# Performance work log

Measured on AMD Instinct MI355X. Metric: run time of the kernel, lower is better.

Reference implementation:

```python
import jax, jax.numpy as jnp
import numpy as np

B, S, IN, E, H, NH = 32, 1024, 16, 128, 256, 4
DH = E // NH
EPS = 1e-5


def _ln(x, g, b):
    mu = jnp.mean(x, axis=-1, keepdims=True)
    var = jnp.mean(jnp.square(x - mu), axis=-1, keepdims=True)
    return (x - mu) * jax.lax.rsqrt(var + EPS) * g + b


def setup_inputs() -> dict:
    key = jax.random.key(0)
    ks = iter(jax.random.split(key, 32))
    n = lambda shape, s=0.02: jax.random.normal(next(ks), shape, jnp.float32) * s
    inp = {
        "x": jax.random.normal(next(ks), (B, S, IN), jnp.float32),
        "mask": jax.random.uniform(next(ks), (B, S), jnp.float32),
        "embed_w": n((E, IN)), "embed_b": jnp.zeros((E,), jnp.float32),
        # 3 encoder layers, params stacked on leading layer axis
        "in_proj_w": n((3, 3 * E, E)), "in_proj_b": jnp.zeros((3, 3 * E), jnp.float32),
        "out_w": n((3, E, E)), "out_b": jnp.zeros((3, E), jnp.float32),
        "ln1_g": jnp.ones((3, E), jnp.float32), "ln1_b": jnp.zeros((3, E), jnp.float32),
        "ln2_g": jnp.ones((3, E), jnp.float32), "ln2_b": jnp.zeros((3, E), jnp.float32),
        "ffn_w1": n((3, E, E)), "ffn_b1": jnp.zeros((3, E), jnp.float32),
        "ffn_w2": n((3, E, E)), "ffn_b2": jnp.zeros((3, E), jnp.float32),
        "cls_w1": n((H, E)), "cls_b1": jnp.zeros((H,), jnp.float32),
        "cls_w2": n((H, H)), "cls_b2": jnp.zeros((H,), jnp.float32),
        "cls_w3": n((H, H)), "cls_b3": jnp.zeros((H,), jnp.float32),
        "cls_w4": n((1, H)), "cls_b4": jnp.zeros((1,), jnp.float32),
    }
    return inp


def _encoder_layer(x, ipw, ipb, ow, ob, g1, b1, g2, b2, w1, fb1, w2, fb2):
    # PyTorch TransformerEncoderLayer, norm_first=False (post-norm), relu FFN
    qkv = x @ ipw.T + ipb                      # [B,S,3E]
    q, k, v = jnp.split(qkv, 3, axis=-1)
    q = q.reshape(B, S, NH, DH).transpose(0, 2, 1, 3)
    k = k.reshape(B, S, NH, DH).transpose(0, 2, 1, 3)
    v = v.reshape(B, S, NH, DH).transpose(0, 2, 1, 3)
    scores = jnp.einsum("bhqd,bhkd->bhqk", q, k) / np.sqrt(DH)  # naive O(S^2) math SDPA
    attn = jax.nn.softmax(scores, axis=-1)
    o = jnp.einsum("bhqk,bhkd->bhqd", attn, v)
    o = o.transpose(0, 2, 1, 3).reshape(B, S, E) @ ow.T + ob
    x = _ln(x + o, g1, b1)
    ff = jax.nn.relu(x @ w1.T + fb1) @ w2.T + fb2
    return _ln(x + ff, g2, b2)


def reference(x, mask, embed_w, embed_b, in_proj_w, in_proj_b, out_w, out_b,
              ln1_g, ln1_b, ln2_g, ln2_b, ffn_w1, ffn_b1, ffn_w2, ffn_b2,
              cls_w1, cls_b1, cls_w2, cls_b2, cls_w3, cls_b3, cls_w4, cls_b4):
    h = jax.nn.relu(x @ embed_w.T + embed_b)   # [B,S,E]
    for i in range(3):
        h = _encoder_layer(h, in_proj_w[i], in_proj_b[i], out_w[i], out_b[i],
                           ln1_g[i], ln1_b[i], ln2_g[i], ln2_b[i],
                           ffn_w1[i], ffn_b1[i], ffn_w2[i], ffn_b2[i])
    pooled = jnp.sum(h * mask[:, :, None], axis=1)  # [B,E] masked sum pool
    z = jax.nn.relu(pooled @ cls_w1.T + cls_b1)
    z = jax.nn.relu(z @ cls_w2.T + cls_b2)
    z = jax.nn.relu(z @ cls_w3.T + cls_b3)
    return jax.nn.sigmoid(z @ cls_w4.T + cls_b4)    # [B,1]
```

## Files before the change

### kernel.cpp

```cpp
#include <hip/hip_runtime.h>
#include <hip/hip_bf16.h>
#include <math.h>

#define B 32
#define S 1024
#define IN_DIM 16
#define E 128
#define NH 4
#define DH 32
#define HDIM 256
#define ROWS (B*S)
#define EPS 1e-5f

#define N_IPW (3*384*128)
#define N_SQ  (3*128*128)
#define NCVT ((N_IPW + 3*N_SQ) / 256)

typedef __bf16 bf16x8 __attribute__((ext_vector_type(8)));
typedef __bf16 bf16x4 __attribute__((ext_vector_type(4)));
typedef __bf16 bf16x2 __attribute__((ext_vector_type(2)));
typedef float f32x4 __attribute__((ext_vector_type(4)));
typedef float f32x16 __attribute__((ext_vector_type(16)));

#define MFMA16 __builtin_amdgcn_mfma_f32_16x16x32_bf16
#define MFMA32 __builtin_amdgcn_mfma_f32_32x32x16_bf16

union BF2U { bf16x2 b; unsigned int u; };
__device__ inline unsigned int pk2(float a, float b) {
    BF2U x; x.b[0] = (__bf16)a; x.b[1] = (__bf16)b; return x.u;
}

union U8 { bf16x8 v8; bf16x4 v4[2]; unsigned u4[4]; };
__device__ inline void st8(__bf16* p, bf16x8 v) {
    U8 u; u.v8 = v;
    *(bf16x4*)p = u.v4[0];
    *(bf16x4*)(p + 4) = u.v4[1];
}
__device__ inline bf16x8 ld8(const __bf16* p) {
    U8 u;
    u.v4[0] = *(const bf16x4*)p;
    u.v4[1] = *(const bf16x4*)(p + 4);
    return u.v8;
}

__global__ __launch_bounds__(256) void k_embedcvt(
        const float* __restrict__ ipw, const float* __restrict__ ow,
        const float* __restrict__ w1, const float* __restrict__ w2,
        __bf16* __restrict__ wbo,
        const float* __restrict__ x, const float* __restrict__ W,
        const float* __restrict__ bias, __bf16* __restrict__ hb)
{
    int t = threadIdx.x;
    if (blockIdx.x < NCVT) {
        int i = blockIdx.x * 256 + t;
        float v;
        if (i < N_IPW) v = ipw[i];
        else if (i < N_IPW + N_SQ) v = ow[i - N_IPW];
        else if (i < N_IPW + 2 * N_SQ) v = w1[i - N_IPW - N_SQ];
        else v = w2[i - N_IPW - 2 * N_SQ];
        wbo[i] = (__bf16)v;
        return;
    }
    int row0 = (blockIdx.x - NCVT) * 16;
    __shared__ float xs[16][16];
    xs[t >> 4][t & 15] = x[(row0 + (t >> 4)) * IN_DIM + (t & 15)];
    __syncthreads();
    int sub = t >> 7, tc = t & 127;
    float w[16];
#pragma unroll
    for (int i = 0; i < 16; ++i) w[i] = W[tc * 16 + i];
    float bb = bias[tc];
#pragma unroll
    for (int rr = 0; rr < 8; ++rr) {
        int lr = sub * 8 + rr;
        float acc = bb;
#pragma unroll
        for (int i = 0; i < 16; ++i) acc += xs[lr][i] * w[i];
        hb[(size_t)(row0 + lr) * E + tc] = (__bf16)fmaxf(acc, 0.f);
    }
}

__global__ __launch_bounds__(512, 2) void k_qkvattn(
        const __bf16* __restrict__ hb, const __bf16* __restrict__ Wip,
        const float* __restrict__ bip, __bf16* __restrict__ O)
{
    __shared__ __attribute__((aligned(16))) __bf16 Ksh[1024][36];
    __shared__ __attribute__((aligned(16))) __bf16 Vsh[32][1036];
    __shared__ __attribute__((aligned(16))) __bf16 Pm[8][32][36];

    int t = threadIdx.x, lane = t & 63, wv = t >> 6;
    int l15 = lane & 15, quad = lane >> 4;
    int l31 = lane & 31, hi = lane >> 5;
    int lb = ((blockIdx.x & 7) << 5) | (blockIdx.x >> 3);
    int half = lb & 1, bh = lb >> 1;
    int hh = bh & 3, b = bh >> 2;

    const __bf16* hpanel = hb + (size_t)b * S * E;

    const float qscale = 0.1767766952966369f * 1.4426950408889634f * 8388608.0f;
    const float C2 = 1065101558.0f;
    f32x16 cinit16, z16;
#pragma unroll
    for (int i = 0; i < 16; ++i) { cinit16[i] = C2; z16[i] = 0.f; }

    bf16x8 bQ[2][2];
    {
        bf16x8 bWq[8];
#pragma unroll
        for (int ch = 0; ch < 8; ++ch)
            bWq[ch] = *(const bf16x8*)&Wip[(size_t)(hh*32 + l31)*128 + ch*16 + hi*8];
        float bq = bip[hh*32 + l31];
#pragma unroll
        for (int qt = 0; qt < 2; ++qt) {
            int qrow0 = half*512 + wv*64 + qt*32;
            f32x16 aq = z16;
#pragma unroll
            for (int ch = 0; ch < 8; ++ch) {
                bf16x8 ah = *(const bf16x8*)&hpanel[(size_t)(qrow0 + l31)*128 + ch*16 + hi*8];
                aq = MFMA32(ah, bWq[ch], aq, 0, 0, 0);
            }
#pragma unroll
            for (int r = 0; r < 16; ++r) {
                int q = (r & 3) + 8*(r >> 2) + 4*hi;
                Pm[wv][q][l31] = (__bf16)((aq[r] + bq) * qscale);
            }
            __asm__ __volatile__("" ::: "memory");
            bQ[qt][0] = ld8(&Pm[wv][l31][hi*8]);
            bQ[qt][1] = ld8(&Pm[wv][l31][16 + hi*8]);
            __asm__ __volatile__("" ::: "memory");
        }
    }

    {
        bf16x8 bWk[2][4], bWv[2][4];
#pragma unroll
        for (int df = 0; df < 2; ++df)
#pragma unroll
            for (int kc = 0; kc < 4; ++kc) {
                bWk[df][kc] = *(const bf16x8*)&Wip[(size_t)(128 + hh*32 + df*16 + l15)*128 + kc*32 + quad*8];
                bWv[df][kc] = *(const bf16x8*)&Wip[(size_t)(256 + hh*32 + df*16 + l15)*128 + kc*32 + quad*8];
            }
        float bk0 = bip[128 + hh*32 + l15],  bk1 = bip[128 + hh*32 + 16 + l15];
        float bvb0 = bip[256 + hh*32 + l15], bvb1 = bip[256 + hh*32 + 16 + l15];
        int srow = wv*16 + l15;
        bf16x8 af[4], ag[4];
#pragma unroll
        for (int kc = 0; kc < 4; ++kc)
            af[kc] = *(const bf16x8*)&hpanel[(size_t)srow*128 + kc*32 + quad*8];
        const f32x4 z4 = {0.f, 0.f, 0.f, 0.f};
        for (int c = 0; c < 8; ++c) {
            if (c < 7) {
#pragma unroll
                for (int kc = 0; kc < 4; ++kc)
                    ag[kc] = *(const bf16x8*)&hpanel[(size_t)((c+1)*128 + srow)*128 + kc*32 + quad*8];
            }
            f32x4 k0 = z4, k1 = z4, v0 = z4, v1 = z4;
#pragma unroll
            for (int kc = 0; kc < 4; ++kc) {
                k0 = MFMA16(af[kc], bWk[0][kc], k0, 0, 0, 0);
                k1 = MFMA16(af[kc], bWk[1][kc], k1, 0, 0, 0);
                v0 = MFMA16(af[kc], bWv[0][kc], v0, 0, 0, 0);
                v1 = MFMA16(af[kc], bWv[1][kc], v1, 0, 0, 0);
            }
            int s0 = c*128 + wv*16 + quad*4;
#pragma unroll
            for (int r = 0; r < 4; ++r) {
                Ksh[s0 + r][l15]      = (__bf16)(k0[r] + bk0);
                Ksh[s0 + r][16 + l15] = (__bf16)(k1[r] + bk1);
            }
            uint2 u0, u1;
            u0.x = pk2(v0[0] + bvb0, v0[1] + bvb0);
            u0.y = pk2(v0[2] + bvb0, v0[3] + bvb0);
            u1.x = pk2(v1[0] + bvb1, v1[1] + bvb1);
            u1.y = pk2(v1[2] + bvb1, v1[3] + bvb1);
            *(uint2*)&Vsh[l15][s0] = u0;
            *(uint2*)&Vsh[16 + l15][s0] = u1;
#pragma unroll
            for (int kc = 0; kc < 4; ++kc) af[kc] = ag[kc];
        }
    }
    __syncthreads();

    bf16x8 vones;
#pragma unroll
    for (int j = 0; j < 8; ++j) vones[j] = (__bf16)1.0f;
    f32x16 o[2], ol[2];
    o[0] = z16; o[1] = z16; ol[0] = z16; ol[1] = z16;

    for (int c = 0; c < 16; ++c) {
        bf16x8 aK[2][2];
#pragma unroll
        for (int sub = 0; sub < 2; ++sub)
#pragma unroll
            for (int dh = 0; dh < 2; ++dh)
                aK[sub][dh] = ld8(&Ksh[c*64 + sub*32 + l31][dh*16 + hi*8]);
        bf16x8 bVf[4];
#pragma unroll
        for (int ch = 0; ch < 4; ++ch) {
            U8 u;
            const __bf16* vp = &Vsh[l31][c*64 + ch*16 + hi*4];
            u.v4[0] = *(const bf16x4*)vp;
            u.v4[1] = *(const bf16x4*)(vp + 8);
            bVf[ch] = u.v8;
        }
#pragma unroll
        for (int qt = 0; qt < 2; ++qt) {
#pragma unroll
            for (int sub = 0; sub < 2; ++sub) {
                f32x16 acc = cinit16;
                acc = MFMA32(aK[sub][0], bQ[qt][0], acc, 0, 0, 0);
                acc = MFMA32(aK[sub][1], bQ[qt][1], acc, 0, 0, 0);
#pragma unroll
                for (int g = 0; g < 2; ++g) {
                    U8 u;
#pragma unroll
                    for (int r = 0; r < 4; ++r) {
                        int ia = (int)acc[g*8 + 2*r];
                        int ib = (int)acc[g*8 + 2*r + 1];
                        u.u4[r] = __builtin_amdgcn_perm((unsigned)ib, (unsigned)ia, 0x07060302u);
                    }
                    bf16x8 ap = u.v8;
                    int ch = sub*2 + g;
                    o[qt]  = MFMA32(ap, bVf[ch], o[qt], 0, 0, 0);
                    ol[qt] = MFMA32(ap, vones,  ol[qt], 0, 0, 0);
                }
            }
        }
    }

#pragma unroll
    for (int qt = 0; qt < 2; ++qt)
#pragma unroll
        for (int r = 0; r < 16; ++r) {
            float linv = 1.f / ol[qt][r];
            int q = (r & 3) + 8*(r >> 2) + 4*hi;
            int row = half*512 + wv*64 + qt*32 + q;
            O[((size_t)(b * S) + row) * E + hh*32 + l31] = (__bf16)(o[qt][r] * linv);
        }
}

__global__ __launch_bounds__(512, 4) void k_layer2(const __bf16* __restrict__ t0b,
        const __bf16* __restrict__ Wo, const float* __restrict__ ob,
        const float* __restrict__ g1, const float* __restrict__ bt1,
        const __bf16* __restrict__ W1, const float* __restrict__ b1v,
        const __bf16* __restrict__ W2, const float* __restrict__ b2v,
        const float* __restrict__ g2, const float* __restrict__ bt2,
        __bf16* __restrict__ hb)
{
    __shared__ __attribute__((aligned(16))) __bf16 As[64][132];
    __shared__ __attribute__((aligned(16))) __bf16 Ws[128][132];
    __shared__ float red[2][64][2];
    int t = threadIdx.x;
    int m0 = blockIdx.x * 64;
    int arow = t >> 3, acol = (t & 7) * 16;
    int wrow = t >> 2, wcol = (t & 3) * 32;
    {
        const __bf16* Ap = t0b + (size_t)(m0 + arow) * 128 + acol;
#pragma unroll
        for (int j = 0; j < 2; ++j)
            st8(&As[arow][acol + j * 8], *(const bf16x8*)&Ap[j * 8]);
        const __bf16* Wp = Wo + (size_t)wrow * 128 + wcol;
#pragma unroll
        for (int j = 0; j < 4; ++j)
            st8(&Ws[wrow][wcol + j * 8], *(const bf16x8*)&Wp[j * 8]);
    }
    __syncthreads();
    int lane = t & 63, wv = t >> 6;
    int l15 = lane & 15, quad = lane >> 4;
    int nh = wv & 1, mh = wv >> 1;
    f32x4 acc[4];

#pragma unroll
    for (int i = 0; i < 4; ++i) acc[i] = (f32x4){0.f, 0.f, 0.f, 0.f};
#pragma unroll
    for (int kc = 0; kc < 4; ++kc) {
        bf16x8 aw[4], ba;
#pragma unroll
        for (int nc = 0; nc < 4; ++nc)
            aw[nc] = ld8(&Ws[nh * 64 + nc * 16 + l15][kc * 32 + quad * 8]);
        ba = ld8(&As[mh * 16 + l15][kc * 32 + quad * 8]);
#pragma unroll
        for (int nc = 0; nc < 4; ++nc)
            acc[nc] = MFMA16(aw[nc], ba, acc[nc], 0, 0, 0);
    }
    float s1 = 0.f, s2 = 0.f;
    int m = m0 + mh * 16 + l15;
#pragma unroll
    for (int nc = 0; nc < 4; ++nc) {
        float4 bv = *(const float4*)&ob[nh * 64 + nc * 16 + quad * 4];
        bf16x4 rv = *(const bf16x4*)&hb[(size_t)m * 128 + nh * 64 + nc * 16 + quad * 4];
        acc[nc][0] += bv.x + (float)rv[0];
        acc[nc][1] += bv.y + (float)rv[1];
        acc[nc][2] += bv.z + (float)rv[2];
        acc[nc][3] += bv.w + (float)rv[3];
#pragma unroll
        for (int i = 0; i < 4; ++i) {
            s1 += acc[nc][i];
            s2 += acc[nc][i] * acc[nc][i];
        }
    }
    s1 += __shfl_xor(s1, 16); s1 += __shfl_xor(s1, 32);
    s2 += __shfl_xor(s2, 16); s2 += __shfl_xor(s2, 32);
    if (quad == 0) {
        red[nh][mh * 16 + l15][0] = s1;
        red[nh][mh * 16 + l15][1] = s2;
    }
    __syncthreads();
    float mu, rs;
    {
        int r = mh * 16 + l15;
        float S1 = red[0][r][0] + red[1][r][0];
        float S2 = red[0][r][1] + red[1][r][1];
        mu = S1 * (1.f / 128.f);
        float var = S2 * (1.f / 128.f) - mu * mu;
        rs = rsqrtf(var + EPS);
    }
    bf16x4 res2[4];
#pragma unroll
    for (int nc = 0; nc < 4; ++nc) {
        float4 gv = *(const float4*)&g1[nh * 64 + nc * 16 + quad * 4];
        float4 bb = *(const float4*)&bt1[nh * 64 + nc * 16 + quad * 4];
        float o0 = (acc[nc][0] - mu) * rs * gv.x + bb.x;
        float o1 = (acc[nc][1] - mu) * rs * gv.y + bb.y;
        float o2 = (acc[nc][2] - mu) * rs * gv.z + bb.z;
        float o3 = (acc[nc][3] - mu) * rs * gv.w + bb.w;
        bf16x4 xb;
        xb[0] = (__bf16)o0; xb[1] = (__bf16)o1;
        xb[2] = (__bf16)o2; xb[3] = (__bf16)o3;
        res2[nc] = xb;
        *(bf16x4*)&As[mh * 16 + l15][nh * 64 + nc * 16 + quad * 4] = xb;
    }
    {
        const __bf16* Wp = W1 + (size_t)wrow * 128 + wcol;
#pragma unroll
        for (int j = 0; j < 4; ++j)
            st8(&Ws[wrow][wcol + j * 8], *(const bf16x8*)&Wp[j * 8]);
    }
    __syncthreads();

#pragma unroll
    for (int i = 0; i < 4; ++i) acc[i] = (f32x4){0.f, 0.f, 0.f, 0.f};
#pragma unroll
    for (int kc = 0; kc < 4; ++kc) {
        bf16x8 aw[4], ba;
#pragma unroll
        for (int nc = 0; nc < 4; ++nc)
            aw[nc] = ld8(&Ws[nh * 64 + nc * 16 + l15][kc * 32 + quad * 8]);
        ba = ld8(&As[mh * 16 + l15][kc * 32 + quad * 8]);
#pragma unroll
        for (int nc = 0; nc < 4; ++nc)
            acc[nc] = MFMA16(aw[nc], ba, acc[nc], 0, 0, 0);
    }
    __syncthreads();
#pragma unroll
    for (int nc = 0; nc < 4; ++nc) {
        float4 bv = *(const float4*)&b1v[nh * 64 + nc * 16 + quad * 4];
        float v0 = fmaxf(acc[nc][0] + bv.x, 0.f);
        float v1 = fmaxf(acc[nc][1] + bv.y, 0.f);
        float v2 = fmaxf(acc[nc][2] + bv.z, 0.f);
        float v3 = fmaxf(acc[nc][3] + bv.w, 0.f);
        uint2 u; u.x = pk2(v0, v1); u.y = pk2(v2, v3);
        *(uint2*)&As[mh * 16 + l15][nh * 64 + nc * 16 + quad * 4] = u;
    }
    {
        const __bf16* Wp = W2 + (size_t)wrow * 128 + wcol;
#pragma unroll
        for (int j = 0; j < 4; ++j)
            st8(&Ws[wrow][wcol + j * 8], *(const bf16x8*)&Wp[j * 8]);
    }
    __syncthreads();

#pragma unroll
    for (int i = 0; i < 4; ++i) acc[i] = (f32x4){0.f, 0.f, 0.f, 0.f};
#pragma unroll
    for (int kc = 0; kc < 4; ++kc) {
        bf16x8 aw[4], ba;
#pragma unroll
        for (int nc = 0; nc < 4; ++nc)
            aw[nc] = ld8(&Ws[nh * 64 + nc * 16 + l15][kc * 32 + quad * 8]);
        ba = ld8(&As[mh * 16 + l15][kc * 32 + quad * 8]);
#pragma unroll
        for (int nc = 0; nc < 4; ++nc)
            acc[nc] = MFMA16(aw[nc], ba, acc[nc], 0, 0, 0);
    }
    s1 = 0.f; s2 = 0.f;
#pragma unroll
    for (int nc = 0; nc < 4; ++nc) {
        float4 bv = *(const float4*)&b2v[nh * 64 + nc * 16 + quad * 4];
        acc[nc][0] += bv.x + (float)res2[nc][0];
        acc[nc][1] += bv.y + (float)res2[nc][1];
        acc[nc][2] += bv.z + (float)res2[nc][2];
        acc[nc][3] += bv.w + (float)res2[nc][3];
#pragma unroll
        for (int i = 0; i < 4; ++i) {
            s1 += acc[nc][i];
            s2 += acc[nc][i] * acc[nc][i];
        }
    }
    s1 += __shfl_xor(s1, 16); s1 += __shfl_xor(s1, 32);
    s2 += __shfl_xor(s2, 16); s2 += __shfl_xor(s2, 32);
    if (quad == 0) {
        red[nh][mh * 16 + l15][0] = s1;
        red[nh][mh * 16 + l15][1] = s2;
    }
    __syncthreads();
    {
        int r = mh * 16 + l15;
        float S1 = red[0][r][0] + red[1][r][0];
        float S2 = red[0][r][1] + red[1][r][1];
        mu = S1 * (1.f / 128.f);
        float var = S2 * (1.f / 128.f) - mu * mu;
        rs = rsqrtf(var + EPS);
    }
#pragma unroll
    for (int nc = 0; nc < 4; ++nc) {
        float4 gv = *(const float4*)&g2[nh * 64 + nc * 16 + quad * 4];
        float4 bb = *(const float4*)&bt2[nh * 64 + nc * 16 + quad * 4];
        float o0 = (acc[nc][0] - mu) * rs * gv.x + bb.x;
        float o1 = (acc[nc][1] - mu) * rs * gv.y + bb.y;
        float o2 = (acc[nc][2] - mu) * rs * gv.z + bb.z;
        float o3 = (acc[nc][3] - mu) * rs * gv.w + bb.w;
        uint2 u; u.x = pk2(o0, o1); u.y = pk2(o2, o3);
        *(uint2*)&hb[(size_t)m * 128 + nh * 64 + nc * 16 + quad * 4] = u;
    }
}

__global__ __launch_bounds__(128) void k_pool1(const __bf16* __restrict__ h,
        const float* __restrict__ mask, float* __restrict__ part)
{
    int bx = blockIdx.x;
    int b = bx >> 3, ch = bx & 7, t = threadIdx.x;
    float acc = 0.f;
    const __bf16* hp = h + (size_t)(b * S + ch * 128) * E + t;
    const float* mp = mask + b * S + ch * 128;
    for (int s = 0; s < 128; ++s) acc += (float)hp[(size_t)s * E] * mp[s];
    part[(size_t)bx * E + t] = acc;
}

__global__ __launch_bounds__(256) void k_head(const float* __restrict__ part,
        const float* __restrict__ cw1, const float* __restrict__ cb1,
        const float* __restrict__ cw2, const float* __restrict__ cb2,
        const float* __restrict__ cw3, const float* __restrict__ cb3,
        const float* __restrict__ cw4, const float* __restrict__ cb4,
        float* __restrict__ out)
{
    int b = blockIdx.x, t = threadIdx.x;
    __shared__ float p[128], za[256], zb[256];
    __shared__ float red4[4];
    if (t < 128) {
        float a = 0.f;
#pragma unroll
        for (int c = 0; c < 8; ++c) a += part[(size_t)(b * 8 + c) * 128 + t];
        p[t] = a;
    }
    __syncthreads();
    float a1 = cb1[t];
    for (int k = 0; k < 128; ++k) a1 += p[k] * cw1[t * 128 + k];
    za[t] = fmaxf(a1, 0.f);
    __syncthreads();
    float a2 = cb2[t];
    for (int k = 0; k < 256; ++k) a2 += za[k] * cw2[t * 256 + k];
    zb[t] = fmaxf(a2, 0.f);
    __syncthreads();
    float a3 = cb3[t];
    for (int k = 0; k < 256; ++k) a3 += zb[k] * cw3[t * 256 + k];
    float z3 = fmaxf(a3, 0.f);
    float prt = z3 * cw4[t];
#pragma unroll
    for (int o2 = 32; o2; o2 >>= 1) prt += __shfl_xor(prt, o2);
    if ((t & 63) == 0) red4[t >> 6] = prt;
    __syncthreads();
    if (t == 0) {
        float sum = red4[0] + red4[1] + red4[2] + red4[3] + cb4[0];
        out[b] = 1.f / (1.f + __expf(-sum));
    }
}

extern "C" void kernel_launch(void* const* d_in, const int* in_sizes, int n_in,
                              void* d_out, int out_size, void* d_ws, size_t ws_size,
                              hipStream_t stream)
{
    const float* x     = (const float*)d_in[0];
    const float* mask  = (const float*)d_in[1];
    const float* emb_w = (const float*)d_in[2];
    const float* emb_b = (const float*)d_in[3];
    const float* ipw   = (const float*)d_in[4];
    const float* ipb   = (const float*)d_in[5];
    const float* ow    = (const float*)d_in[6];
    const float* ob    = (const float*)d_in[7];
    const float* ln1g  = (const float*)d_in[8];
    const float* ln1b  = (const float*)d_in[9];
    const float* ln2g  = (const float*)d_in[10];
    const float* ln2b  = (const float*)d_in[11];
    const float* w1    = (const float*)d_in[12];
    const float* fb1   = (const float*)d_in[13];
    const float* w2    = (const float*)d_in[14];
    const float* fb2   = (const float*)d_in[15];
    const float* cw1   = (const float*)d_in[16];
    const float* cb1   = (const float*)d_in[17];
    const float* cw2   = (const float*)d_in[18];
    const float* cb2   = (const float*)d_in[19];
    const float* cw3   = (const float*)d_in[20];
    const float* cb3   = (const float*)d_in[21];
    const float* cw4   = (const float*)d_in[22];
    const float* cb4   = (const float*)d_in[23];

    char* p = (char*)d_ws;
    __bf16* hb   = (__bf16*)p;   p += (size_t)ROWS * E * 2;
    p += (size_t)ROWS * 256 * 2;
    p += (size_t)ROWS * 32 * 4 * 2 / 4;
    __bf16* t0b  = (__bf16*)p;   p += (size_t)ROWS * E * 2;
    __bf16* wb   = (__bf16*)p;   p += (size_t)(N_IPW + 3 * N_SQ) * 2;
    float* part  = (float*)p;    p += (size_t)B * 8 * E * 4;

    __bf16* wb_ipw = wb;
    __bf16* wb_ow  = wb + N_IPW;
    __bf16* wb_w1  = wb_ow + N_SQ;
    __bf16* wb_w2  = wb_w1 + N_SQ;

    k_embedcvt<<<NCVT + ROWS / 16, 256, 0, stream>>>(
        ipw, ow, w1, w2, wb, x, emb_w, emb_b, hb);
    for (int L = 0; L < 3; ++L) {
        k_qkvattn<<<B * NH * 2, 512, 0, stream>>>(
            hb, wb_ipw + (size_t)L * 384 * 128, ipb + L * 384, t0b);
        k_layer2<<<ROWS / 64, 512, 0, stream>>>(
            t0b, wb_ow + (size_t)L * 128 * 128, ob + L * 128,
            ln1g + L * E, ln1b + L * E,
            wb_w1 + (size_t)L * 128 * 128, fb1 + L * 128,
            wb_w2 + (size_t)L * 128 * 128, fb2 + L * 128,
            ln2g + L * E, ln2b + L * E, hb);
    }
    k_pool1<<<B * 8, 128, 0, stream>>>(hb, mask, part);
    k_head<<<B, 256, 0, stream>>>(part, cw1, cb1, cw2, cb2, cw3, cb3, cw4, cb4,
                                  (float*)d_out);
}
```

Before: 291.7 us.

## Double attention block threads, one query tile per wave, scalar row sums

The attention kernel now launches 1024 threads per block. Each of the 16 waves owns a single 32-row query tile instead of two, and the K/V projection loop splits across twice as many waves. The row-sum MFMA against a ones vector is replaced by a scalar accumulation of the probabilities plus a cross-lane shuffle and a small shared scratch. The Q staging buffer now reuses the Ksh region, which adds a barrier. The pooling kernel is vectorised with 8-wide bf16 loads and a shared-memory reduction. This trades per-wave register pressure and MFMA work for more waves per CU, with a risk of occupancy limits from the 1024-thread launch bound.

```diff
diff --git a/kernel.cpp b/kernel.cpp
--- a/kernel.cpp
+++ b/kernel.cpp
@@ -80,13 +80,13 @@
     }
 }
 
-__global__ __launch_bounds__(512, 2) void k_qkvattn(
+__global__ __launch_bounds__(1024, 4) void k_qkvattn(
         const __bf16* __restrict__ hb, const __bf16* __restrict__ Wip,
         const float* __restrict__ bip, __bf16* __restrict__ O)
 {
     __shared__ __attribute__((aligned(16))) __bf16 Ksh[1024][36];
     __shared__ __attribute__((aligned(16))) __bf16 Vsh[32][1036];
-    __shared__ __attribute__((aligned(16))) __bf16 Pm[8][32][36];
+    __shared__ float lscr[16][32];
 
     int t = threadIdx.x, lane = t & 63, wv = t >> 6;
     int l15 = lane & 15, quad = lane >> 4;
@@ -103,33 +103,32 @@
 #pragma unroll
     for (int i = 0; i < 16; ++i) { cinit16[i] = C2; z16[i] = 0.f; }
 
-    bf16x8 bQ[2][2];
+    bf16x8 bQ[2];
     {
         bf16x8 bWq[8];
 #pragma unroll
         for (int ch = 0; ch < 8; ++ch)
             bWq[ch] = *(const bf16x8*)&Wip[(size_t)(hh*32 + l31)*128 + ch*16 + hi*8];
         float bq = bip[hh*32 + l31];
-#pragma unroll
-        for (int qt = 0; qt < 2; ++qt) {
-            int qrow0 = half*512 + wv*64 + qt*32;
-            f32x16 aq = z16;
-#pragma unroll
-            for (int ch = 0; ch < 8; ++ch) {
-                bf16x8 ah = *(const bf16x8*)&hpanel[(size_t)(qrow0 + l31)*128 + ch*16 + hi*8];
-                aq = MFMA32(ah, bWq[ch], aq, 0, 0, 0);
-            }
-#pragma unroll
-            for (int r = 0; r < 16; ++r) {
-                int q = (r & 3) + 8*(r >> 2) + 4*hi;
-                Pm[wv][q][l31] = (__bf16)((aq[r] + bq) * qscale);
-            }
-            __asm__ __volatile__("" ::: "memory");
-            bQ[qt][0] = ld8(&Pm[wv][l31][hi*8]);
-            bQ[qt][1] = ld8(&Pm[wv][l31][16 + hi*8]);
-            __asm__ __volatile__("" ::: "memory");
-        }
-    }
+        int qrow0 = half*512 + wv*32;
+        f32x16 aq = z16;
+#pragma unroll
+        for (int ch = 0; ch < 8; ++ch) {
+            bf16x8 ah = *(const bf16x8*)&hpanel[(size_t)(qrow0 + l31)*128 + ch*16 + hi*8];
+            aq = MFMA32(ah, bWq[ch], aq, 0, 0, 0);
+        }
+        __bf16* PmS = &Ksh[wv*32][0];
+#pragma unroll
+        for (int r = 0; r < 16; ++r) {
+            int q = (r & 3) + 8*(r >> 2) + 4*hi;
+            PmS[q*36 + l31] = (__bf16)((aq[r] + bq) * qscale);
+        }
+        __asm__ __volatile__("" ::: "memory");
+        bQ[0] = ld8(&PmS[l31*36 + hi*8]);
+        bQ[1] = ld8(&PmS[l31*36 + 16 + hi*8]);
+        __asm__ __volatile__("" ::: "memory");
+    }
+    __syncthreads();
 
     {
         bf16x8 bWk[2][4], bWv[2][4];
@@ -148,11 +147,11 @@
         for (int kc = 0; kc < 4; ++kc)
             af[kc] = *(const bf16x8*)&hpanel[(size_t)srow*128 + kc*32 + quad*8];
         const f32x4 z4 = {0.f, 0.f, 0.f, 0.f};
-        for (int c = 0; c < 8; ++c) {
-            if (c < 7) {
+        for (int c = 0; c < 4; ++c) {
+            if (c < 3) {
 #pragma unroll
                 for (int kc = 0; kc < 4; ++kc)
-                    ag[kc] = *(const bf16x8*)&hpanel[(size_t)((c+1)*128 + srow)*128 + kc*32 + quad*8];
+                    ag[kc] = *(const bf16x8*)&hpanel[(size_t)((c+1)*256 + srow)*128 + kc*32 + quad*8];
             }
             f32x4 k0 = z4, k1 = z4, v0 = z4, v1 = z4;
 #pragma unroll
@@ -162,7 +161,7 @@
                 v0 = MFMA16(af[kc], bWv[0][kc], v0, 0, 0, 0);
                 v1 = MFMA16(af[kc], bWv[1][kc], v1, 0, 0, 0);
             }
-            int s0 = c*128 + wv*16 + quad*4;
+            int s0 = c*256 + wv*16 + quad*4;
 #pragma unroll
             for (int r = 0; r < 4; ++r) {
                 Ksh[s0 + r][l15]      = (__bf16)(k0[r] + bk0);
@@ -181,11 +180,8 @@
     }
     __syncthreads();
 
-    bf16x8 vones;
-#pragma unroll
-    for (int j = 0; j < 8; ++j) vones[j] = (__bf16)1.0f;
-    f32x16 o[2], ol[2];
-    o[0] = z16; o[1] = z16; ol[0] = z16; ol[1] = z16;
+    f32x16 o = z16;
+    float lsum = 0.f;
 
     for (int c = 0; c < 16; ++c) {
         bf16x8 aK[2][2];
@@ -204,39 +200,36 @@
             bVf[ch] = u.v8;
         }
 #pragma unroll
-        for (int qt = 0; qt < 2; ++qt) {
-#pragma unroll
-            for (int sub = 0; sub < 2; ++sub) {
-                f32x16 acc = cinit16;
-                acc = MFMA32(aK[sub][0], bQ[qt][0], acc, 0, 0, 0);
-                acc = MFMA32(aK[sub][1], bQ[qt][1], acc, 0, 0, 0);
-#pragma unroll
-                for (int g = 0; g < 2; ++g) {
-                    U8 u;
-#pragma unroll
-                    for (int r = 0; r < 4; ++r) {
-                        int ia = (int)acc[g*8 + 2*r];
-                        int ib = (int)acc[g*8 + 2*r + 1];
-                        u.u4[r] = __builtin_amdgcn_perm((unsigned)ib, (unsigned)ia, 0x07060302u);
-                    }
-                    bf16x8 ap = u.v8;
-                    int ch = sub*2 + g;
-                    o[qt]  = MFMA32(ap, bVf[ch], o[qt], 0, 0, 0);
-                    ol[qt] = MFMA32(ap, vones,  ol[qt], 0, 0, 0);
+        for (int sub = 0; sub < 2; ++sub) {
+            f32x16 acc = cinit16;
+            acc = MFMA32(aK[sub][0], bQ[0], acc, 0, 0, 0);
+            acc = MFMA32(aK[sub][1], bQ[1], acc, 0, 0, 0);
+#pragma unroll
+            for (int g = 0; g < 2; ++g) {
+                U8 u;
+#pragma unroll
+                for (int r = 0; r < 4; ++r) {
+                    int ia = (int)acc[g*8 + 2*r];
+                    int ib = (int)acc[g*8 + 2*r + 1];
+                    u.u4[r] = __builtin_amdgcn_perm((unsigned)ib, (unsigned)ia, 0x07060302u);
+                    lsum += __int_as_float(ia) + __int_as_float(ib);
                 }
+                o = MFMA32(u.v8, bVf[sub*2 + g], o, 0, 0, 0);
             }
         }
     }
 
-#pragma unroll
-    for (int qt = 0; qt < 2; ++qt)
-#pragma unroll
-        for (int r = 0; r < 16; ++r) {
-            float linv = 1.f / ol[qt][r];
-            int q = (r & 3) + 8*(r >> 2) + 4*hi;
-            int row = half*512 + wv*64 + qt*32 + q;
-            O[((size_t)(b * S) + row) * E + hh*32 + l31] = (__bf16)(o[qt][r] * linv);
-        }
+    lsum += __shfl_xor(lsum, 32);
+    float linv = 1.f / lsum;
+    if (hi == 0) lscr[wv][l31] = linv;
+    __asm__ __volatile__("" ::: "memory");
+#pragma unroll
+    for (int r = 0; r < 16; ++r) {
+        int q = (r & 3) + 8*(r >> 2) + 4*hi;
+        float li = lscr[wv][q];
+        int row = half*512 + wv*32 + q;
+        O[((size_t)(b * S) + row) * E + hh*32 + l31] = (__bf16)(o[r] * li);
+    }
 }
 
 __global__ __launch_bounds__(512, 4) void k_layer2(const __bf16* __restrict__ t0b,
@@ -425,16 +418,34 @@
     }
 }
 
-__global__ __launch_bounds__(128) void k_pool1(const __bf16* __restrict__ h,
+__global__ __launch_bounds__(256) void k_pool1(const __bf16* __restrict__ h,
         const float* __restrict__ mask, float* __restrict__ part)
 {
     int bx = blockIdx.x;
     int b = bx >> 3, ch = bx & 7, t = threadIdx.x;
-    float acc = 0.f;
-    const __bf16* hp = h + (size_t)(b * S + ch * 128) * E + t;
-    const float* mp = mask + b * S + ch * 128;
-    for (int s = 0; s < 128; ++s) acc += (float)hp[(size_t)s * E] * mp[s];
-    part[(size_t)bx * E + t] = acc;
+    int sg = t >> 4, cg = t & 15;
+    __shared__ float red[16][128];
+    float acc[8];
+#pragma unroll
+    for (int j = 0; j < 8; ++j) acc[j] = 0.f;
+    const __bf16* hp = h + ((size_t)(b * S + ch * 128 + sg)) * E + cg * 8;
+    const float* mp = mask + b * S + ch * 128 + sg;
+#pragma unroll
+    for (int k = 0; k < 8; ++k) {
+        float m = mp[k * 16];
+        bf16x8 hv = *(const bf16x8*)&hp[(size_t)(k * 16) * E];
+#pragma unroll
+        for (int j = 0; j < 8; ++j) acc[j] += (float)hv[j] * m;
+    }
+#pragma unroll
+    for (int j = 0; j < 8; ++j) red[sg][cg * 8 + j] = acc[j];
+    __syncthreads();
+    if (t < 128) {
+        float a = 0.f;
+#pragma unroll
+        for (int sgi = 0; sgi < 16; ++sgi) a += red[sgi][t];
+        part[(size_t)bx * E + t] = a;
+    }
 }
 
 __global__ __launch_bounds__(256) void k_head(const float* __restrict__ part,
@@ -521,7 +532,7 @@
     k_embedcvt<<<NCVT + ROWS / 16, 256, 0, stream>>>(
         ipw, ow, w1, w2, wb, x, emb_w, emb_b, hb);
     for (int L = 0; L < 3; ++L) {
-        k_qkvattn<<<B * NH * 2, 512, 0, stream>>>(
+        k_qkvattn<<<B * NH * 2, 1024, 0, stream>>>(
             hb, wb_ipw + (size_t)L * 384 * 128, ipb + L * 384, t0b);
         k_layer2<<<ROWS / 64, 512, 0, stream>>>(
             t0b, wb_ow + (size_t)L * 128 * 128, ob + L * 128,
@@ -530,7 +541,7 @@
             wb_w2 + (size_t)L * 128 * 128, fb2 + L * 128,
             ln2g + L * E, ln2b + L * E, hb);
     }
-    k_pool1<<<B * 8, 128, 0, stream>>>(hb, mask, part);
+    k_pool1<<<B * 8, 256, 0, stream>>>(hb, mask, part);
     k_head<<<B, 256, 0, stream>>>(part, cw1, cb1, cw2, cb2, cw3, cb3, cw4, cb4,
                                   (float*)d_out);
 }
```

Measured after the change: 306.5 us. 1.05x slower.
